# Performance work log

Measured on AMD Instinct MI355X. Metric: run time of the kernel, lower is better.

## Reference

```python
import jax, jax.numpy as jnp
import numpy as np
from jax import lax

B, T, H, W = 4, 8, 14, 14
DIM, NH = 768, 8
HD = DIM // NH            # 96, head dim (= depthwise conv channels)
G = 1                     # global_embed_num
N = T * H * W + 1 + G     # 1570 tokens: [global, cls, spatial]
HID = 4 * DIM
BIG = 1.0e8


def ln(x, g, b, eps=1e-5):
    m = jnp.mean(x, axis=-1, keepdims=True)
    v = jnp.mean(jnp.square(x - m), axis=-1, keepdims=True)
    return (x - m) * jax.lax.rsqrt(v + eps) * g + b


def setup_inputs() -> dict:
    key = jax.random.key(0)
    ks = jax.random.split(key, 12)
    s = 0.02
    inp = {
        "x": jax.random.normal(ks[0], (B, N, DIM), jnp.float32),
        "t": T, "h": H, "w": W,
        "norm1_g": jnp.ones((DIM,), jnp.float32),
        "norm1_b": jnp.zeros((DIM,), jnp.float32),
        "qkv_w": jax.random.normal(ks[1], (3 * DIM, DIM), jnp.float32) * s,
        "qkv_b": jnp.zeros((3 * DIM,), jnp.float32),
        "conv_q": jax.random.normal(ks[2], (HD, 1, 3, 3, 3), jnp.float32) * 0.05,
        "nq_g": jnp.ones((HD,), jnp.float32), "nq_b": jnp.zeros((HD,), jnp.float32),
        "conv_k": jax.random.normal(ks[3], (HD, 1, 3, 3, 3), jnp.float32) * 0.05,
        "nk_g": jnp.ones((HD,), jnp.float32), "nk_b": jnp.zeros((HD,), jnp.float32),
        "conv_v": jax.random.normal(ks[4], (HD, 1, 3, 3, 3), jnp.float32) * 0.05,
        "nv_g": jnp.ones((HD,), jnp.float32), "nv_b": jnp.zeros((HD,), jnp.float32),
        "proj_w": jax.random.normal(ks[5], (DIM, DIM), jnp.float32) * s,
        "proj_b": jnp.zeros((DIM,), jnp.float32),
        "norm2_g": jnp.ones((DIM,), jnp.float32),
        "norm2_b": jnp.zeros((DIM,), jnp.float32),
        "fc1_w": jax.random.normal(ks[6], (HID, DIM), jnp.float32) * s,
        "fc1_b": jnp.zeros((HID,), jnp.float32),
        "fc2_w": jax.random.normal(ks[7], (DIM, HID), jnp.float32) * s,
        "fc2_b": jnp.zeros((DIM,), jnp.float32),
    }
    return inp


def _pool(tok, cw, g, b):
    # tok: [B, NH, N, HD] -> depthwise conv3d per head on spatial tokens, then LN
    glob, cls, body = tok[:, :, :G], tok[:, :, G:G + 1], tok[:, :, G + 1:]
    z = body.reshape(B * NH, T, H, W, HD).transpose(0, 4, 1, 2, 3)  # [BN, C, T, H, W]
    z = lax.conv_general_dilated(z, cw, window_strides=(1, 1, 1),
                                 padding=[(1, 1)] * 3, feature_group_count=HD,
                                 dimension_numbers=("NCDHW", "OIDHW", "NCDHW"))
    z = z.reshape(B, NH, HD, T * H * W).transpose(0, 1, 3, 2)       # [B, NH, L, HD]
    z = jnp.concatenate([glob, cls, z], axis=2)                     # splice cls then global
    return ln(z, g, b)


def reference(x, t, h, w, norm1_g, norm1_b, qkv_w, qkv_b,
              conv_q, nq_g, nq_b, conv_k, nk_g, nk_b, conv_v, nv_g, nv_b,
              proj_w, proj_b, norm2_g, norm2_b, fc1_w, fc1_b, fc2_w, fc2_b):
    scale = HD ** (-0.5)
    xn = ln(x, norm1_g, norm1_b)
    qkv = (xn @ qkv_w.T + qkv_b).reshape(B, N, 3, NH, HD)
    qkv = qkv.transpose(2, 0, 3, 1, 4)            # [3, B, NH, N, HD]
    q = _pool(qkv[0], conv_q, nq_g, nq_b)
    k = _pool(qkv[1], conv_k, nk_g, nk_b)
    v = _pool(qkv[2], conv_v, nv_g, nv_b)

    attn = jnp.einsum("bhnd,bhmd->bhnm", q, k) * scale
    # additive offset: BIG everywhere except diagonal and the global columns (rows >= G)
    eye = jnp.eye(N, dtype=attn.dtype)
    off2 = eye * BIG
    off2 = off2.at[G:, :G].set(BIG)
    offset = BIG - off2                            # [N, N]
    attn = jax.nn.softmax(attn - offset, axis=-1)

    o = jnp.einsum("bhnm,bhmd->bhnd", attn, v)     # [B, NH, N, HD]
    o = o.transpose(0, 2, 1, 3).reshape(B, N, DIM)
    o = o @ proj_w.T + proj_b

    x = x + o                                      # pool_skip is None -> identity skip
    x2 = ln(x, norm2_g, norm2_b)
    mlp = jax.nn.gelu(x2 @ fc1_w.T + fc1_b, approximate=False) @ fc2_w.T + fc2_b
    return x + mlp
```

## Files before the change

### kernel.cpp

```cpp
#include <hip/hip_runtime.h>
#include <hip/hip_bf16.h>
#include <cmath>

using bf16 = __hip_bfloat16;
using bf16x8_t = __attribute__((ext_vector_type(8))) short;
using f32x4_t  = __attribute__((ext_vector_type(4))) float;

constexpr int kT = 8;
constexpr int kDIM = 768, kNH = 8, kHD = 96;
constexpr int kN = 1570;
constexpr int kB = 4;
constexpr int kM = kB * kN;
constexpr int kBNH = kB * kNH;
constexpr long kPoolRows  = (long)kBNH * kN;
constexpr long kPoolElems = kPoolRows * kHD;

struct SegTab { const void* src[22]; long start[23]; };

__global__ void detect_kernel(const unsigned* __restrict__ probe,
                              unsigned* __restrict__ flag) {
  *flag = (probe[0] == 0x3F803F80u) ? 1u : 0u;
}

__global__ void convert_kernel(SegTab tab, bf16* __restrict__ cin,
                               const unsigned* __restrict__ flag, long chunks) {
  const bool isb = (*flag != 0u);
  const long stride = (long)gridDim.x * blockDim.x;
  for (long c = (long)blockIdx.x * blockDim.x + threadIdx.x; c < chunks; c += stride) {
    const long e8 = c * 8;
    int lo = 0, hi = 22;
    while (hi - lo > 1) { int mid = (lo + hi) >> 1; if (e8 >= tab.start[mid]) lo = mid; else hi = mid; }
    const long e = e8 - tab.start[lo];
    if (isb) {
      *(bf16x8_t*)(cin + e8) = *(const bf16x8_t*)((const unsigned short*)tab.src[lo] + e);
    } else {
      const float* s = (const float*)tab.src[lo] + e;
      float4 a = *(const float4*)s;
      float4 b = *(const float4*)(s + 4);
      bf16 r[8];
      r[0] = (bf16)a.x; r[1] = (bf16)a.y; r[2] = (bf16)a.z; r[3] = (bf16)a.w;
      r[4] = (bf16)b.x; r[5] = (bf16)b.y; r[6] = (bf16)b.z; r[7] = (bf16)b.w;
      *(bf16x8_t*)(cin + e8) = *(bf16x8_t*)r;
    }
  }
}

__device__ __forceinline__ void gload_lds16(const bf16* g, bf16* l) {
  __builtin_amdgcn_global_load_lds(
      (const __attribute__((address_space(1))) unsigned int*)g,
      (__attribute__((address_space(3))) unsigned int*)l, 16, 0, 0);
}

template<int EPI, int DUAL>
__launch_bounds__(256, 2)
__global__ void gemm_bt(const bf16* __restrict__ A, const bf16* __restrict__ Wt,
                        const bf16* __restrict__ bias, const bf16* __restrict__ res,
                        bf16* __restrict__ C, float* __restrict__ Cf,
                        const unsigned* __restrict__ flagp,
                        int M, int K, int Nout, int tiles_n)
{
  __shared__ bf16 As[2][128 * 64];
  __shared__ bf16 Bs[2][128 * 64];
  const int tid  = threadIdx.x;
  const int lane = tid & 63;
  const int wv   = tid >> 6;
  const int wr   = wv >> 1, wc = wv & 1;

  const int nwg = gridDim.x;
  const int q = nwg >> 3, rr = nwg & 7;
  const int xcd = blockIdx.x & 7, slot = blockIdx.x >> 3;
  const int base = (xcd < rr) ? xcd * (q + 1) : rr * (q + 1) + (xcd - rr) * q;
  const int lin = base + slot;
  const long tile_m = (long)(lin / tiles_n) * 128;
  const long tile_n = (long)(lin % tiles_n) * 128;

  bool isb = true;
  if constexpr (DUAL) isb = (*flagp != 0u);

  f32x4_t zero = {0.f, 0.f, 0.f, 0.f};
  f32x4_t acc[4][4];
#pragma unroll
  for (int i = 0; i < 4; ++i)
#pragma unroll
    for (int j = 0; j < 4; ++j) acc[i][j] = zero;

  const int rbase = tid >> 3;
  const int g8 = (((tid & 7) ^ (rbase & 7))) * 8;
  const bf16* srcA[4];
  const bf16* srcB[4];
#pragma unroll
  for (int i = 0; i < 4; ++i) {
    long ar = tile_m + i * 32 + rbase; if (ar > M - 1) ar = M - 1;
    srcA[i] = A  + ar * K + g8;
    srcB[i] = Wt + (tile_n + i * 32 + rbase) * K + g8;
  }

  const int rsel = lane & 15;
  const int qq = lane & 7;
  const int j0 = (((lane >> 4) ^ qq)) * 8;
  const int j1 = (((lane >> 4) ^ 4 ^ qq)) * 8;
  const int rowA0 = wr * 64 + rsel;
  const int rowB0 = wc * 64 + rsel;

  auto stage = [&](int kt, int buf) {
    const long koff = (long)kt << 6;
#pragma unroll
    for (int i = 0; i < 4; ++i)
      gload_lds16(srcA[i] + koff, &As[buf][i * 2048 + wv * 512]);
#pragma unroll
    for (int i = 0; i < 4; ++i)
      gload_lds16(srcB[i] + koff, &Bs[buf][i * 2048 + wv * 512]);
  };

  const int ksteps = K >> 6;
  stage(0, 0);
  stage(1, 1);
  asm volatile("s_waitcnt vmcnt(8)" ::: "memory");
  __builtin_amdgcn_s_barrier();

  int cur = 0;
  for (int kt = 0; kt < ksteps; ++kt) {
    bf16x8_t a[4][2], b[4][2];
#pragma unroll
    for (int m = 0; m < 4; ++m) {
      const int ra = (rowA0 + m * 16) << 6;
      a[m][0] = *(const bf16x8_t*)&As[cur][ra + j0];
      a[m][1] = *(const bf16x8_t*)&As[cur][ra + j1];
      const int rb = (rowB0 + m * 16) << 6;
      b[m][0] = *(const bf16x8_t*)&Bs[cur][rb + j0];
      b[m][1] = *(const bf16x8_t*)&Bs[cur][rb + j1];
    }
    asm volatile("s_waitcnt lgkmcnt(0)" ::: "memory");
    __builtin_amdgcn_sched_barrier(0);
    __builtin_amdgcn_s_barrier();
    const bool pf = (kt + 2 < ksteps);
    if (pf) stage(kt + 2, cur);
#pragma unroll
    for (int m = 0; m < 4; ++m)
#pragma unroll
      for (int n = 0; n < 4; ++n) {
        acc[m][n] = __builtin_amdgcn_mfma_f32_16x16x32_bf16(a[m][0], b[n][0], acc[m][n], 0, 0, 0);
        acc[m][n] = __builtin_amdgcn_mfma_f32_16x16x32_bf16(a[m][1], b[n][1], acc[m][n], 0, 0, 0);
      }
    if (pf) asm volatile("s_waitcnt vmcnt(8)" ::: "memory");
    else    asm volatile("s_waitcnt vmcnt(0)" ::: "memory");
    __builtin_amdgcn_s_barrier();
    cur ^= 1;
  }

  const long colBase = tile_n + wc * 64 + (lane & 15);
  const long rowBase = tile_m + wr * 64 + ((lane >> 4) << 2);
#pragma unroll
  for (int n = 0; n < 4; ++n) {
    const long col = colBase + n * 16;
    const float bv = (float)bias[col];
#pragma unroll
    for (int m = 0; m < 4; ++m) {
      const long row0 = rowBase + m * 16;
#pragma unroll
      for (int r = 0; r < 4; ++r) {
        const long row = row0 + r;
        if (row < M) {
          float v2 = acc[m][n][r] + bv;
          if constexpr (EPI == 1) {
            v2 = 0.5f * v2 * (1.f + erff(v2 * 0.70710678118654752f));
          } else if constexpr (EPI == 2) {
            v2 += (float)res[row * Nout + col];
          }
          if constexpr (DUAL) {
            if (isb) C[row * Nout + col] = (bf16)v2;
            else     Cf[row * Nout + col] = v2;
          } else {
            C[row * Nout + col] = (bf16)v2;
          }
        }
      }
    }
  }
}

__global__ void ln768_kernel(const bf16* __restrict__ x, const bf16* __restrict__ g,
                             const bf16* __restrict__ bta, bf16* __restrict__ y)
{
  const long row = blockIdx.x;
  const int tid = threadIdx.x;
  const bf16* xr = x + row * kDIM;
  float v[3];
  float s = 0.f, ss = 0.f;
#pragma unroll
  for (int i = 0; i < 3; ++i) {
    v[i] = (float)xr[tid + i * 256];
    s += v[i]; ss += v[i] * v[i];
  }
#pragma unroll
  for (int off = 32; off; off >>= 1) {
    s  += __shfl_xor(s, off);
    ss += __shfl_xor(ss, off);
  }
  __shared__ float red[8];
  const int wv = tid >> 6;
  if ((tid & 63) == 0) { red[wv] = s; red[4 + wv] = ss; }
  __syncthreads();
  s  = red[0] + red[1] + red[2] + red[3];
  ss = red[4] + red[5] + red[6] + red[7];
  const float mean = s * (1.f / kDIM);
  const float var  = ss * (1.f / kDIM) - mean * mean;
  const float rstd = rsqrtf(var + 1e-5f);
  bf16* yr = y + row * kDIM;
#pragma unroll
  for (int i = 0; i < 3; ++i) {
    const int c = tid + i * 256;
    yr[c] = (bf16)((v[i] - mean) * rstd * (float)g[c] + (float)bta[c]);
  }
}

__launch_bounds__(256, 2)
__global__ void convpool2_kernel(const bf16* __restrict__ qkv,
                                 const bf16* __restrict__ cwq,
                                 const bf16* __restrict__ cwk,
                                 const bf16* __restrict__ cwv,
                                 bf16* __restrict__ pool)
{
  __shared__ bf16 tile[3 * 256 * 40];
  const int t    = blockIdx.x;
  const int bh   = blockIdx.y;
  const int z    = blockIdx.z;
  const int s    = z / 3, cgrp = z - s * 3;
  const int tid  = threadIdx.x;
  const int b    = bh >> 3, h = bh & 7;

  const bf16* src0 = qkv + (long)(b * kN) * 2304 + s * kDIM + h * kHD + cgrp * 32;

  {
    f32x4_t z4 = {0.f, 0.f, 0.f, 0.f};
    for (int i = tid; i < 3840; i += 256)
      *(f32x4_t*)((char*)tile + (long)i * 16) = z4;
  }
  __syncthreads();

  for (int c = tid; c < 2352; c += 256) {
    const int slice = c / 784;
    const int rem   = c - slice * 784;
    const int p     = rem >> 2;
    const int seg   = rem & 3;
    const int tt    = t + slice - 1;
    if ((unsigned)tt < 8u) {
      const int y = p / 14, x = p - y * 14;
      const int n = 2 + tt * 196 + p;
      const bf16x8_t v = *(const bf16x8_t*)(src0 + (long)n * 2304 + seg * 8);
      *(bf16x8_t*)((char*)tile + ((long)(slice * 256 + (y + 1) * 16 + (x + 1)) * 40 + seg * 8) * 2) = v;
    }
  }

  const int dpair = tid & 15;
  const int pg    = tid >> 4;
  const int d0    = cgrp * 32 + dpair * 2;
  const bf16* cw  = (s == 0) ? cwq : (s == 1) ? cwk : cwv;
  float w0[27], w1[27];
#pragma unroll
  for (int i = 0; i < 27; ++i) {
    w0[i] = (float)cw[d0 * 27 + i];
    w1[i] = (float)cw[(d0 + 1) * 27 + i];
  }
  __syncthreads();

  bf16* out0 = pool + (long)s * kPoolElems + (long)bh * kN * kHD;
  for (int p = pg; p < 196; p += 16) {
    const int y = p / 14, x = p - y * 14;
    const char* bp = (const char*)tile + ((long)(y * 16 + x) * 40 + dpair * 2) * 2;
    float a0 = 0.f, a1 = 0.f;
#pragma unroll
    for (int dt = 0; dt < 3; ++dt)
#pragma unroll
      for (int dy = 0; dy < 3; ++dy)
#pragma unroll
        for (int dx = 0; dx < 3; ++dx) {
          const unsigned u = *(const unsigned*)(bp + dt * 20480 + dy * 1280 + dx * 80);
          const int i = (dt * 3 + dy) * 3 + dx;
          a0 = fmaf(__uint_as_float(u << 16), w0[i], a0);
          a1 = fmaf(__uint_as_float(u & 0xffff0000u), w1[i], a1);
        }
    const int n = 2 + t * 196 + p;
    bf16 r0 = (bf16)a0, r1 = (bf16)a1;
    unsigned pk = ((unsigned)*(unsigned short*)&r1 << 16) | *(unsigned short*)&r0;
    *(unsigned*)((char*)(out0 + (long)n * kHD + d0)) = pk;
  }
  if (t == 0 && tid < 64) {
    const int tok = tid >> 5, dd = tid & 31;
    out0[(long)tok * kHD + cgrp * 32 + dd] = src0[(long)tok * 2304 + dd];
  }
}

__global__ void ln96_kernel(bf16* __restrict__ pool,
                            const bf16* __restrict__ gq, const bf16* __restrict__ bq,
                            const bf16* __restrict__ gk, const bf16* __restrict__ bk,
                            const bf16* __restrict__ gv, const bf16* __restrict__ bv)
{
  const int z = blockIdx.y;
  bf16* buf = pool + (long)z * kPoolElems;
  const bf16* g  = (z == 0) ? gq : (z == 1) ? gk : gv;
  const bf16* be = (z == 0) ? bq : (z == 1) ? bk : bv;
  const long row = (long)blockIdx.x * 4 + (threadIdx.x >> 6);
  if (row >= kPoolRows) return;
  const int lane = threadIdx.x & 63;
  bf16* p = buf + row * kHD;
  float a0 = 0.f, a1 = 0.f;
  if (lane < 48) {
    a0 = (float)p[lane * 2];
    a1 = (float)p[lane * 2 + 1];
  }
  float sSum = a0 + a1, sSq = a0 * a0 + a1 * a1;
#pragma unroll
  for (int off = 32; off; off >>= 1) {
    sSum += __shfl_xor(sSum, off);
    sSq  += __shfl_xor(sSq, off);
  }
  const float mean = sSum * (1.f / 96);
  const float var  = sSq * (1.f / 96) - mean * mean;
  const float rstd = rsqrtf(var + 1e-5f);
  if (lane < 48) {
    p[lane * 2]     = (bf16)((a0 - mean) * rstd * (float)g[lane * 2]     + (float)be[lane * 2]);
    p[lane * 2 + 1] = (bf16)((a1 - mean) * rstd * (float)g[lane * 2 + 1] + (float)be[lane * 2 + 1]);
  }
}

__global__ void attn_kernel(const bf16* __restrict__ pool, bf16* __restrict__ o)
{
  const long idx = (long)blockIdx.x * 4 + (threadIdx.x >> 6);
  if (idx >= kPoolRows) return;
  const int bh = (int)(idx / kN);
  const int i  = (int)(idx - (long)bh * kN);
  const int lane = threadIdx.x & 63;
  const bf16* qrow  = pool + ((long)bh * kN + i) * kHD;
  const bf16* kbase = pool + kPoolElems + (long)bh * kN * kHD;
  const bf16* vbase = pool + 2 * kPoolElems + (long)bh * kN * kHD;
  float q0 = 0, q1 = 0, ki0 = 0, ki1 = 0, k00 = 0, k01 = 0;
  float vi0 = 0, vi1 = 0, v00 = 0, v01 = 0;
  if (lane < 48) {
    const int c = lane * 2;
    q0  = (float)qrow[c];                  q1  = (float)qrow[c + 1];
    ki0 = (float)kbase[(long)i * kHD + c]; ki1 = (float)kbase[(long)i * kHD + c + 1];
    k00 = (float)kbase[c];                 k01 = (float)kbase[c + 1];
    vi0 = (float)vbase[(long)i * kHD + c]; vi1 = (float)vbase[(long)i * kHD + c + 1];
    v00 = (float)vbase[c];                 v01 = (float)vbase[c + 1];
  }
  float ds = q0 * ki0 + q1 * ki1;
  float dg = q0 * k00 + q1 * k01;
#pragma unroll
  for (int off = 32; off; off >>= 1) {
    ds += __shfl_xor(ds, off);
    dg += __shfl_xor(dg, off);
  }
  float o0, o1;
  if (i == 0) { o0 = v00; o1 = v01; }
  else {
    const float scale = 0.10206207261596575f;
    const float l0 = dg * scale, li = ds * scale;
    const float mx = fmaxf(l0, li);
    const float e0 = __expf(l0 - mx), ei = __expf(li - mx);
    const float inv = 1.f / (e0 + ei);
    o0 = (e0 * v00 + ei * vi0) * inv;
    o1 = (e0 * v01 + ei * vi1) * inv;
  }
  if (lane < 48) {
    const int b = bh >> 3, h = bh & 7;
    bf16* orow = o + ((long)b * kN + i) * kDIM + h * kHD + lane * 2;
    orow[0] = (bf16)o0;
    orow[1] = (bf16)o1;
  }
}

extern "C" void kernel_launch(void* const* d_in, const int* in_sizes, int n_in,
                              void* d_out, int out_size, void* d_ws, size_t ws_size,
                              hipStream_t stream)
{
  const int map[22] = {0,4,5,6,7,8,9,10,11,12,13,14,15,16,17,18,19,20,21,22,23,24};

  char* ws = (char*)d_ws;
  unsigned* flag = (unsigned*)ws;

  size_t off = 256;
  auto take = [&](size_t bytes) {
    size_t r = off;
    off += (bytes + 255) & ~(size_t)255;
    return r;
  };

  SegTab tab;
  long total = 0;
  tab.start[0] = 0;
  for (int j = 0; j < 22; ++j) {
    tab.src[j] = d_in[map[j]];
    total += in_sizes[map[j]];
    tab.start[j + 1] = total;
  }

  bf16* cin = (bf16*)(ws + take((size_t)total * 2));

  bf16* cp[22];
  { long acc = 0;
    for (int j = 0; j < 22; ++j) { cp[j] = cin + acc; acc += in_sizes[map[j]]; } }
  bf16* x_c    = cp[0];
  bf16* n1g_c  = cp[1],  *n1b_c = cp[2];
  bf16* qkvw_c = cp[3],  *qkvb_c = cp[4];
  bf16* cwq_c  = cp[5],  *nqg_c = cp[6],  *nqb_c = cp[7];
  bf16* cwk_c  = cp[8],  *nkg_c = cp[9],  *nkb_c = cp[10];
  bf16* cwv_c  = cp[11], *nvg_c = cp[12], *nvb_c = cp[13];
  bf16* projw_c = cp[14], *projb_c = cp[15];
  bf16* n2g_c  = cp[16], *n2b_c = cp[17];
  bf16* fc1w_c = cp[18], *fc1b_c = cp[19];
  bf16* fc2w_c = cp[20], *fc2b_c = cp[21];

  bf16* qkv  = (bf16*)(ws + take(38584320));
  bf16* xn   = (bf16*)(ws + take(9646080));
  bf16* pool = (bf16*)(ws + take(28938240));
  bf16* x1   = (bf16*)(ws + take(9646080));
  bf16* o   = xn;
  bf16* h1  = qkv;
  bf16* x2n = pool;

  bf16*  out_b = (bf16*)d_out;
  float* out_f = (float*)d_out;

  detect_kernel<<<1, 1, 0, stream>>>((const unsigned*)d_in[4], flag);
  convert_kernel<<<2048, 256, 0, stream>>>(tab, cin, flag, total / 8);

  ln768_kernel<<<kM, 256, 0, stream>>>(x_c, n1g_c, n1b_c, xn);
  gemm_bt<0,0><<<50 * 18, 256, 0, stream>>>(xn, qkvw_c, qkvb_c, nullptr, qkv, nullptr, nullptr, kM, 768, 2304, 18);
  convpool2_kernel<<<dim3(kT, kBNH, 9), 256, 0, stream>>>(qkv, cwq_c, cwk_c, cwv_c, pool);
  ln96_kernel<<<dim3((int)((kPoolRows + 3) / 4), 3), 256, 0, stream>>>(pool, nqg_c, nqb_c, nkg_c, nkb_c, nvg_c, nvb_c);
  attn_kernel<<<(int)((kPoolRows + 3) / 4), 256, 0, stream>>>(pool, o);
  gemm_bt<2,0><<<50 * 6, 256, 0, stream>>>(o, projw_c, projb_c, x_c, x1, nullptr, nullptr, kM, 768, 768, 6);
  ln768_kernel<<<kM, 256, 0, stream>>>(x1, n2g_c, n2b_c, x2n);
  gemm_bt<1,0><<<50 * 24, 256, 0, stream>>>(x2n, fc1w_c, fc1b_c, nullptr, h1, nullptr, nullptr, kM, 768, 3072, 24);
  gemm_bt<2,1><<<50 * 6, 256, 0, stream>>>(h1, fc2w_c, fc2b_c, x1, out_b, out_f, flag, kM, 3072, 768, 6);
}
```

Before: 314.9 us.

## Stage GEMM epilogue through LDS with vectorized stores, fast GELU, tile swizzle

The GEMM epilogue now writes accumulators plus bias to LDS, then reads them back as 8-wide chunks for coalesced 16-byte global stores and residual loads. Exact erf GELU is replaced with a tanh-style sigmoid approximation using exp and rcp. Tiles are remapped so pairs of M tiles share N ordering for better cache reuse. The k-loop is unrolled by two with priority raising around MFMAs. The trade-off is extra bf16 rounding before the residual add and a GELU approximation error.

```diff
diff --git a/kernel.cpp b/kernel.cpp
--- a/kernel.cpp
+++ b/kernel.cpp
@@ -59,20 +59,21 @@
                         const unsigned* __restrict__ flagp,
                         int M, int K, int Nout, int tiles_n)
 {
-  __shared__ bf16 As[2][128 * 64];
-  __shared__ bf16 Bs[2][128 * 64];
+  __shared__ bf16 shm[32768];
   const int tid  = threadIdx.x;
   const int lane = tid & 63;
   const int wv   = tid >> 6;
   const int wr   = wv >> 1, wc = wv & 1;
 
   const int nwg = gridDim.x;
-  const int q = nwg >> 3, rr = nwg & 7;
+  const int q8 = nwg >> 3, r8 = nwg & 7;
   const int xcd = blockIdx.x & 7, slot = blockIdx.x >> 3;
-  const int base = (xcd < rr) ? xcd * (q + 1) : rr * (q + 1) + (xcd - rr) * q;
+  const int base = (xcd < r8) ? xcd * (q8 + 1) : r8 * (q8 + 1) + (xcd - r8) * q8;
   const int lin = base + slot;
-  const long tile_m = (long)(lin / tiles_n) * 128;
-  const long tile_n = (long)(lin % tiles_n) * 128;
+  const int grp = lin / (2 * tiles_n);
+  const int rem = lin - grp * 2 * tiles_n;
+  const long tile_m = (long)(grp * 2 + (rem & 1)) * 128;
+  const long tile_n = (long)(rem >> 1) * 128;
 
   bool isb = true;
   if constexpr (DUAL) isb = (*flagp != 0u);
@@ -95,22 +96,23 @@
     srcB[i] = Wt + (tile_n + i * 32 + rbase) * K + g8;
   }
 
-  const int rsel = lane & 15;
+  auto stage = [&](int kt, int buf) {
+    const long koff = (long)kt << 6;
+    bf16* ab = shm + buf * 8192;
+    bf16* bp = shm + 16384 + buf * 8192;
+#pragma unroll
+    for (int i = 0; i < 4; ++i)
+      gload_lds16(srcA[i] + koff, ab + i * 2048 + wv * 512);
+#pragma unroll
+    for (int i = 0; i < 4; ++i)
+      gload_lds16(srcB[i] + koff, bp + i * 2048 + wv * 512);
+  };
+
   const int qq = lane & 7;
   const int j0 = (((lane >> 4) ^ qq)) * 8;
   const int j1 = (((lane >> 4) ^ 4 ^ qq)) * 8;
-  const int rowA0 = wr * 64 + rsel;
-  const int rowB0 = wc * 64 + rsel;
-
-  auto stage = [&](int kt, int buf) {
-    const long koff = (long)kt << 6;
-#pragma unroll
-    for (int i = 0; i < 4; ++i)
-      gload_lds16(srcA[i] + koff, &As[buf][i * 2048 + wv * 512]);
-#pragma unroll
-    for (int i = 0; i < 4; ++i)
-      gload_lds16(srcB[i] + koff, &Bs[buf][i * 2048 + wv * 512]);
-  };
+  const int rA = wr * 64 + (lane & 15);
+  const int rB = wc * 64 + (lane & 15);
 
   const int ksteps = K >> 6;
   stage(0, 0);
@@ -118,62 +120,97 @@
   asm volatile("s_waitcnt vmcnt(8)" ::: "memory");
   __builtin_amdgcn_s_barrier();
 
-  int cur = 0;
-  for (int kt = 0; kt < ksteps; ++kt) {
-    bf16x8_t a[4][2], b[4][2];
-#pragma unroll
-    for (int m = 0; m < 4; ++m) {
-      const int ra = (rowA0 + m * 16) << 6;
-      a[m][0] = *(const bf16x8_t*)&As[cur][ra + j0];
-      a[m][1] = *(const bf16x8_t*)&As[cur][ra + j1];
-      const int rb = (rowB0 + m * 16) << 6;
-      b[m][0] = *(const bf16x8_t*)&Bs[cur][rb + j0];
-      b[m][1] = *(const bf16x8_t*)&Bs[cur][rb + j1];
+#define KSTEP(BUF, DOPF, PFKT)                                                 \
+  {                                                                            \
+    const bf16* ab = shm + (BUF) * 8192;                                       \
+    const bf16* bp = shm + 16384 + (BUF) * 8192;                               \
+    bf16x8_t a[4][2], bfr[4][2];                                               \
+    _Pragma("unroll")                                                          \
+    for (int m = 0; m < 4; ++m) {                                              \
+      a[m][0]   = *(const bf16x8_t*)&ab[((rA + m * 16) << 6) + j0];            \
+      a[m][1]   = *(const bf16x8_t*)&ab[((rA + m * 16) << 6) + j1];            \
+      bfr[m][0] = *(const bf16x8_t*)&bp[((rB + m * 16) << 6) + j0];            \
+      bfr[m][1] = *(const bf16x8_t*)&bp[((rB + m * 16) << 6) + j1];            \
+    }                                                                          \
+    asm volatile("s_waitcnt lgkmcnt(0)" ::: "memory");                         \
+    __builtin_amdgcn_sched_barrier(0);                                         \
+    __builtin_amdgcn_s_barrier();                                              \
+    if (DOPF) stage((PFKT), (BUF));                                            \
+    __builtin_amdgcn_s_setprio(1);                                             \
+    _Pragma("unroll")                                                          \
+    for (int m = 0; m < 4; ++m)                                                \
+      _Pragma("unroll")                                                        \
+      for (int n = 0; n < 4; ++n) {                                            \
+        acc[m][n] = __builtin_amdgcn_mfma_f32_16x16x32_bf16(a[m][0], bfr[n][0], acc[m][n], 0, 0, 0); \
+        acc[m][n] = __builtin_amdgcn_mfma_f32_16x16x32_bf16(a[m][1], bfr[n][1], acc[m][n], 0, 0, 0); \
+      }                                                                        \
+    __builtin_amdgcn_s_setprio(0);                                             \
+    if (DOPF) { asm volatile("s_waitcnt vmcnt(8)" ::: "memory"); }             \
+    else      { asm volatile("s_waitcnt vmcnt(0)" ::: "memory"); }             \
+    __builtin_amdgcn_s_barrier();                                              \
+  }
+
+  for (int p = 0; p < ksteps; p += 2) {
+    KSTEP(0, p + 2 < ksteps, p + 2)
+    KSTEP(1, p + 3 < ksteps, p + 3)
+  }
+#undef KSTEP
+
+  {
+    const int colB = wc * 64 + (lane & 15);
+    const int rowB = wr * 64 + ((lane >> 4) << 2);
+#pragma unroll
+    for (int n = 0; n < 4; ++n) {
+      const int col = colB + n * 16;
+      const float bv = (float)bias[tile_n + col];
+#pragma unroll
+      for (int m = 0; m < 4; ++m)
+#pragma unroll
+        for (int r = 0; r < 4; ++r)
+          shm[(rowB + m * 16 + r) * 136 + col] = (bf16)(acc[m][n][r] + bv);
     }
-    asm volatile("s_waitcnt lgkmcnt(0)" ::: "memory");
-    __builtin_amdgcn_sched_barrier(0);
-    __builtin_amdgcn_s_barrier();
-    const bool pf = (kt + 2 < ksteps);
-    if (pf) stage(kt + 2, cur);
-#pragma unroll
-    for (int m = 0; m < 4; ++m)
-#pragma unroll
-      for (int n = 0; n < 4; ++n) {
-        acc[m][n] = __builtin_amdgcn_mfma_f32_16x16x32_bf16(a[m][0], b[n][0], acc[m][n], 0, 0, 0);
-        acc[m][n] = __builtin_amdgcn_mfma_f32_16x16x32_bf16(a[m][1], b[n][1], acc[m][n], 0, 0, 0);
+  }
+  __syncthreads();
+#pragma unroll
+  for (int c8 = 0; c8 < 8; ++c8) {
+    const int chunk = tid + c8 * 256;
+    const int row = chunk >> 4;
+    const int colc = (chunk & 15) * 8;
+    const long grow = tile_m + row;
+    if (grow < M) {
+      const bf16x8_t v8 = *(const bf16x8_t*)&shm[row * 136 + colc];
+      const long gcol = tile_n + colc;
+      float f[8];
+#pragma unroll
+      for (int j = 0; j < 8; ++j) {
+        unsigned short u = (unsigned short)v8[j];
+        f[j] = __uint_as_float((unsigned)u << 16);
       }
-    if (pf) asm volatile("s_waitcnt vmcnt(8)" ::: "memory");
-    else    asm volatile("s_waitcnt vmcnt(0)" ::: "memory");
-    __builtin_amdgcn_s_barrier();
-    cur ^= 1;
-  }
-
-  const long colBase = tile_n + wc * 64 + (lane & 15);
-  const long rowBase = tile_m + wr * 64 + ((lane >> 4) << 2);
-#pragma unroll
-  for (int n = 0; n < 4; ++n) {
-    const long col = colBase + n * 16;
-    const float bv = (float)bias[col];
-#pragma unroll
-    for (int m = 0; m < 4; ++m) {
-      const long row0 = rowBase + m * 16;
-#pragma unroll
-      for (int r = 0; r < 4; ++r) {
-        const long row = row0 + r;
-        if (row < M) {
-          float v2 = acc[m][n][r] + bv;
-          if constexpr (EPI == 1) {
-            v2 = 0.5f * v2 * (1.f + erff(v2 * 0.70710678118654752f));
-          } else if constexpr (EPI == 2) {
-            v2 += (float)res[row * Nout + col];
-          }
-          if constexpr (DUAL) {
-            if (isb) C[row * Nout + col] = (bf16)v2;
-            else     Cf[row * Nout + col] = v2;
-          } else {
-            C[row * Nout + col] = (bf16)v2;
-          }
+      if constexpr (EPI == 1) {
+#pragma unroll
+        for (int j = 0; j < 8; ++j) {
+          const float v2 = f[j];
+          const float zarg = 1.59576912160573f * v2 * (1.f + 0.044715f * v2 * v2);
+          f[j] = v2 * __builtin_amdgcn_rcpf(1.f + __expf(-zarg));
         }
+      } else if constexpr (EPI == 2) {
+        const bf16x8_t rv = *(const bf16x8_t*)&res[grow * Nout + gcol];
+#pragma unroll
+        for (int j = 0; j < 8; ++j) {
+          unsigned short u = (unsigned short)rv[j];
+          f[j] += __uint_as_float((unsigned)u << 16);
+        }
+      }
+      if (DUAL && !isb) {
+        float4 s0 = {f[0], f[1], f[2], f[3]};
+        float4 s1 = {f[4], f[5], f[6], f[7]};
+        *(float4*)&Cf[grow * Nout + gcol] = s0;
+        *(float4*)&Cf[grow * Nout + gcol + 4] = s1;
+      } else {
+        bf16 o8[8];
+#pragma unroll
+        for (int j = 0; j < 8; ++j) o8[j] = (bf16)f[j];
+        *(bf16x8_t*)&C[grow * Nout + gcol] = *(bf16x8_t*)o8;
       }
     }
   }
```

Result: faster. 281.1 us (-10.7%).
